# Performance work log

Hardware: AMD Instinct MI355X
Metric: run time of the kernel (lower is better)

The kernel has to match this reference:

```python
import jax, jax.numpy as jnp
import numpy as np

BLANK = 0
SIZE_AVERAGE = True


def rnnt_loss(acts, labels, act_lens, label_lens):
    # acts: (B, T, U+1, V) raw logits; warp-transducer applies log_softmax internally
    B, T, U1, V = acts.shape
    U = U1 - 1
    logp = jax.nn.log_softmax(acts, axis=-1)          # (B,T,U1,V)
    lp_blank = logp[..., BLANK]                       # (B,T,U1)
    # emission log-prob of label u at grid point (t,u): logp[b,t,u,labels[b,u]]
    lp_emit = jnp.take_along_axis(
        logp[:, :, :U, :], labels[:, None, :, None].astype(jnp.int32), axis=3
    )[..., 0]                                         # (B,T,U)

    # alpha[0,0]=0 ; alpha[0,u] = sum_{k<u} emit[0,k]
    row0 = jnp.concatenate(
        [jnp.zeros((B, 1), acts.dtype), jnp.cumsum(lp_emit[:, 0, :], axis=1)], axis=1
    )                                                 # (B,U1)

    def outer(prev_row, xs):
        blank_prev, emit_t = xs                       # (B,U1), (B,U)
        fb = prev_row + blank_prev                    # arrive via blank from t-1
        def inner(carry, x):
            fb_u, em_prev = x                         # (B,), (B,)
            a = jnp.logaddexp(fb_u, carry + em_prev)  # blank vs emit path
            return a, a
        _, rest = jax.lax.scan(inner, fb[:, 0], (fb[:, 1:].T, emit_t.T))  # (U,B)
        row = jnp.concatenate([fb[:, :1], rest.T], axis=1)               # (B,U1)
        return row, row

    xs = (jnp.moveaxis(lp_blank[:, :-1, :], 1, 0),   # (T-1,B,U1)
          jnp.moveaxis(lp_emit[:, 1:, :], 1, 0))     # (T-1,B,U)
    _, rows = jax.lax.scan(outer, row0, xs)          # (T-1,B,U1)
    alpha = jnp.concatenate([row0[None], rows], axis=0)  # (T,B,U1)

    b_idx = jnp.arange(B)
    t_idx = act_lens.astype(jnp.int32) - 1
    u_idx = label_lens.astype(jnp.int32)
    loglike = alpha[t_idx, b_idx, u_idx] + lp_blank[b_idx, t_idx, u_idx]
    total = -jnp.sum(loglike)
    if SIZE_AVERAGE:
        total = total / B
    return total.reshape(1)


def setup_inputs() -> dict:
    key = jax.random.key(0)
    k1, k2, k3, k4 = jax.random.split(key, 4)
    B, T, U, V = 8, 256, 100, 128
    acts = jax.random.normal(k1, (B, T, U + 1, V), dtype=jnp.float32)
    labels = jax.random.randint(k2, (B, U), 0, V, dtype=jnp.int64)
    act_lens = jax.random.randint(k3, (B,), T // 2, T + 1, dtype=jnp.int32)
    label_lens = jax.random.randint(k4, (B,), U // 2, U + 1, dtype=jnp.int32)
    return {"acts": acts, "labels": labels, "act_lens": act_lens, "label_lens": label_lens}


def reference(acts, labels, act_lens, label_lens):
    return rnnt_loss(acts, labels, act_lens, label_lens)
```

## Files before the change

### kernel.cpp

```cpp
#include <hip/hip_runtime.h>
#include <math.h>


#define B_DIM  8
#define T_DIM  256
#define U_DIM  100
#define U1_DIM 101
#define V_DIM  128

#define ROWU   128
#define DROWS  360
#define NEGF   (-8.0e29f)
#define LOG2E  1.4426950408889634f
#define LN2    0.69314718055994530942f

#define NITMAX 88
#define VROWU  320
#define VROWB  1280
#define LDS_BYTES (NITMAX * VROWB)

typedef unsigned uv2 __attribute__((ext_vector_type(2)));

__device__ __forceinline__ float ubit(unsigned u) { return __builtin_bit_cast(float, u); }
__device__ __forceinline__ float logadd2(float a, float b) {
    float m = fmaxf(a, b);
    float e = exp2f(-fabsf(a - b));
    return m + log2f(1.0f + e);
}
__device__ __forceinline__ float lse3(float a, float b, float c) {
    float m = fmaxf(fmaxf(a, b), c);
    float s = exp2f(a - m) + exp2f(b - m) + exp2f(c - m);
    return m + log2f(s);
}
__device__ __forceinline__ float lse5(float a, float b, float c, float d, float e) {
    float m = fmaxf(fmaxf(fmaxf(a, b), c), fmaxf(d, e));
    float s = exp2f(a - m) + exp2f(b - m) + exp2f(c - m) + exp2f(d - m) + exp2f(e - m);
    return m + log2f(s);
}
__device__ __forceinline__ float lane_shr1(float x) {
    int r = __builtin_amdgcn_update_dpp(0, __builtin_bit_cast(int, x),
                                        0x138 , 0xF, 0xF, true);
    return __builtin_bit_cast(float, r);
}
__device__ __forceinline__ unsigned f2bf(float f) {
    unsigned u = __builtin_bit_cast(unsigned, f);
    u += 0x7FFF + ((u >> 16) & 1);
    return u >> 16;
}

struct W2 { float tA, mA, lA, tB, mB, lB; };
__device__ __forceinline__ W2 buildW2m(uv2 c0, uv2 cm, int l, int d, int tl, int ul) {
    const int ua = 2 * l, ub = 2 * l + 1;
    float BL0a = ubit(c0.x << 16), EM0a = ubit(c0.x & 0xFFFF0000u);
    float BL0b = ubit(c0.y << 16), EM0b = ubit(c0.y & 0xFFFF0000u);
    float BLma = ubit(cm.x << 16), EMma = ubit(cm.x & 0xFFFF0000u);
    float BLmb = ubit(cm.y << 16), EMmb = ubit(cm.y & 0xFFFF0000u);
    BL0a = (ua <= ul && (unsigned)(d - 1 - ua) <= (unsigned)tl) ? BL0a : NEGF;
    BL0b = (ub <= ul && (unsigned)(d - 1 - ub) <= (unsigned)tl) ? BL0b : NEGF;
    EM0a = (ua >= 1 && ua <= ul && (unsigned)(d - ua) <= (unsigned)tl) ? EM0a : NEGF;
    EM0b = (ub <= ul && (unsigned)(d - ub) <= (unsigned)tl) ? EM0b : NEGF;
    BLma = (ua <= ul && (unsigned)(d - 2 - ua) <= (unsigned)tl) ? BLma : NEGF;
    BLmb = (ub <= ul && (unsigned)(d - 1 - ub) <= (unsigned)tl) ? BLmb : NEGF;
    EMma = (ua >= 1 && ua <= ul && (unsigned)(d - 1 - ua) <= (unsigned)tl) ? EMma : NEGF;
    EMmb = (ub <= ul && (unsigned)(d - 1 - ub) <= (unsigned)tl) ? EMmb : NEGF;
    float BLmp = lane_shr1(BLmb), EMmp = lane_shr1(EMmb);
    W2 w;
    w.tA = BLma + BL0a;
    w.mA = logadd2(EMma + BL0a, BLmp + EM0a);
    w.lA = EMmp + EM0a;
    w.tB = BLmb + BL0b;
    w.mB = logadd2(EMmb + BL0b, BLma + EM0b);
    w.lB = EMma + EM0b;
    if (l == 0) { w.mA = NEGF; w.lA = NEGF; w.lB = NEGF; }
    return w;
}

__device__ __forceinline__ void buildV4(const unsigned* combB, int dt, int l,
                                        int tl, int ul, float* out) {
    const unsigned* C = combB + (size_t)dt * ROWU + 2 * l;
    uv2 c0 = *(const uv2*)(C);
    uv2 c1 = *(const uv2*)(C - ROWU);
    uv2 c2 = *(const uv2*)(C - 2 * ROWU);
    uv2 c3 = *(const uv2*)(C - 3 * ROWU);
    W2 P = buildW2m(c0, c1, l, dt,     tl, ul);
    W2 Q = buildW2m(c2, c3, l, dt - 2, tl, ul);
    float Qt_b1 = lane_shr1(Q.tB), Qm_b1 = lane_shr1(Q.mB), Ql_b1 = lane_shr1(Q.lB);
    float Qt_a1 = lane_shr1(Q.tA), Qm_a1 = lane_shr1(Q.mA), Ql_a1 = lane_shr1(Q.lA);
    out[0] = P.tA + Q.tA;
    out[1] = logadd2(P.tA + Q.mA, P.mA + Qt_b1);
    out[2] = lse3(P.tA + Q.lA, P.mA + Qm_b1, P.lA + Qt_a1);
    out[3] = logadd2(P.mA + Ql_b1, P.lA + Qm_a1);
    out[4] = P.lA + Ql_a1;
    out[5] = P.tB + Q.tB;
    out[6] = logadd2(P.tB + Q.mB, P.mB + Q.tA);
    out[7] = lse3(P.tB + Q.lB, P.mB + Q.mA, P.lB + Qt_b1);
    out[8] = logadd2(P.mB + Q.lA, P.lB + Qm_b1);
    out[9] = P.lB + Ql_b1;
    if (l == 0) { out[1] = NEGF; out[2] = NEGF; out[3] = NEGF; out[4] = NEGF; }
}

__device__ __forceinline__ void prologue(const unsigned* combB, int start, int l,
                                         int tl, int ul, float& v0, float& v1) {
    v0 = (l == 0) ? 0.0f : NEGF;
    v1 = NEGF;
    for (int d = 1; d <= start; ++d) {
        uv2 c = *(const uv2*)(combB + (size_t)d * ROWU + 2 * l);
        const int ua = 2 * l, ub = 2 * l + 1;
        float bl0 = ubit(c.x << 16), em0 = ubit(c.x & 0xFFFF0000u);
        float bl1 = ubit(c.y << 16), em1 = ubit(c.y & 0xFFFF0000u);
        bl0 = (ua <= ul && (unsigned)(d - 1 - ua) <= (unsigned)tl) ? bl0 : NEGF;
        bl1 = (ub <= ul && (unsigned)(d - 1 - ub) <= (unsigned)tl) ? bl1 : NEGF;
        em0 = (ua >= 1 && ua <= ul && (unsigned)(d - ua) <= (unsigned)tl) ? em0 : NEGF;
        em1 = (ub <= ul && (unsigned)(d - ub) <= (unsigned)tl) ? em1 : NEGF;
        float left0 = lane_shr1(v1);
        float a0 = v0 + bl0, p0 = left0 + em0;
        float a1 = v1 + bl1, p1 = v0 + em1;
        v0 = logadd2(a0, p0);
        v1 = logadd2(a1, p1);
    }
}

__global__ __launch_bounds__(256) void lsm_kernel(
    const float* __restrict__ acts, const int* __restrict__ labels,
    const int* __restrict__ act_lens, const int* __restrict__ label_lens,
    unsigned short* __restrict__ comb, int* __restrict__ counter, int nrows)
{
    if (blockIdx.x == 0 && threadIdx.x == 0) *counter = 0;

    int rid = blockIdx.x * 8 + (threadIdx.x >> 5);
    if (rid >= nrows) return;
    int hl = threadIdx.x & 31;

    int u  = rid % U1_DIM;
    int bt = rid / U1_DIM;
    int b  = bt / T_DIM;
    int t  = bt - b * T_DIM;
    if (t >= act_lens[b] || u > label_lens[b]) return;

    const float* row = acts + (size_t)rid * V_DIM;
    float4 x = *reinterpret_cast<const float4*>(row + 4 * hl);
    float4 y = make_float4(x.x * LOG2E, x.y * LOG2E, x.z * LOG2E, x.w * LOG2E);

    float s = exp2f(y.x) + exp2f(y.y) + exp2f(y.z) + exp2f(y.w);
    #pragma unroll
    for (int off = 16; off; off >>= 1) s += __shfl_xor(s, off);
    float lse2 = log2f(s);

    unsigned short* C = comb + (size_t)b * DROWS * (ROWU * 2);
    int d = t + u + 1;
    if (hl == 0)
        C[(size_t)d * (ROWU * 2) + 2 * u] = (unsigned short)f2bf(y.x - lse2);
    if (u < U_DIM) {
        int lab = labels[b * U_DIM + u];
        if (hl == (lab >> 2)) {
            int r = lab & 3;
            float v = (r == 0) ? y.x : (r == 1) ? y.y : (r == 2) ? y.z : y.w;
            C[(size_t)d * (ROWU * 2) + 2 * u + 3] = (unsigned short)f2bf(v - lse2);
        }
    }
}

__global__ __launch_bounds__(256) void v4c_kernel(
    const unsigned* __restrict__ comb,
    const int* __restrict__ act_lens, const int* __restrict__ label_lens,
    unsigned* __restrict__ V)
{
    int wid = blockIdx.x * 4 + (threadIdx.x >> 6);
    if (wid >= B_DIM * NITMAX) return;
    int l  = threadIdx.x & 63;
    int b  = wid / NITMAX;
    int it = wid - b * NITMAX;

    int tl = act_lens[b] - 1, ul = label_lens[b];
    int dfin = tl + ul, start = dfin & 3, niter = dfin >> 2;
    if (it >= niter) return;
    int dt = start + 4 * (it + 1);

    float o[10];
    buildV4(comb + (size_t)b * DROWS * ROWU, dt, l, tl, ul, o);

    if (l < 52) {
        unsigned* ro = V + (size_t)(b * NITMAX + it) * VROWU;
        uv2 p0, p1, p2;
        p0.x = f2bf(o[0]) | (f2bf(o[1]) << 16); p0.y = f2bf(o[5]) | (f2bf(o[6]) << 16);
        p1.x = f2bf(o[2]) | (f2bf(o[3]) << 16); p1.y = f2bf(o[7]) | (f2bf(o[8]) << 16);
        p2.x = f2bf(o[4]);                      p2.y = f2bf(o[9]);
        __builtin_nontemporal_store(p0, (uv2*)(ro + 2 * l));
        __builtin_nontemporal_store(p1, (uv2*)(ro + 104 + 2 * l));
        __builtin_nontemporal_store(p2, (uv2*)(ro + 208 + 2 * l));
    }
}

__global__ __launch_bounds__(64, 1) void dp3_kernel(
    const unsigned* __restrict__ comb, const unsigned* __restrict__ V,
    const int* __restrict__ act_lens, const int* __restrict__ label_lens,
    float* __restrict__ loglike, int* __restrict__ counter,
    float* __restrict__ out)
{
    extern __shared__ char sV[];

    const int b = blockIdx.x;
    const int l = threadIdx.x;
    const int tl    = act_lens[b] - 1;
    const int ul    = label_lens[b];
    const int dfin  = tl + ul;
    const int start = dfin & 3;
    const int niter = dfin >> 2;

    const unsigned* combB = comb + (size_t)b * DROWS * ROWU;

    float fin_bl = ubit(combB[(size_t)(dfin + 1) * ROWU + ul] << 16);
    float v0, v1;
    prologue(combB, start, l, tl, ul, v0, v1);
    asm volatile("s_waitcnt vmcnt(0)" ::: "memory");

    {
        const char* g = (const char*)(V + (size_t)b * NITMAX * VROWU) + l * 16;
        const int nload = (niter * VROWB + 1023) >> 10;
        for (int i = 0; i < nload; ++i) {
            __builtin_amdgcn_global_load_lds(
                (const __attribute__((address_space(1))) void*)(g + (size_t)i * 1024),
                (__attribute__((address_space(3))) void*)(sV + (size_t)i * 1024), 16, 0, 0);
        }
        asm volatile("s_waitcnt vmcnt(0)" ::: "memory");
    }

    float rf0 = NEGF, rf1 = NEGF;
    const char* Lc = sV + 8 * l;
    uv2 q0[4], q1[4], q2[4];
    #pragma unroll
    for (int j = 0; j < 4; ++j) {
        const char* p = Lc + (size_t)j * VROWB;
        q0[j] = *(const uv2*)(p);
        q1[j] = *(const uv2*)(p + 416);
        q2[j] = *(const uv2*)(p + 832);
    }
    const int ngroups = (niter + 3) >> 2;
    for (int g4 = 0; g4 < ngroups; ++g4) {
        const int it0 = g4 * 4;
        #pragma unroll
        for (int J = 0; J < 4; ++J) {
            const int it = it0 + J;
            uv2 a0 = q0[J], a1 = q1[J], a2 = q2[J];
            float V0a = ubit(a0.x << 16), V1a = ubit(a0.x & 0xFFFF0000u);
            float V0b = ubit(a0.y << 16), V1b = ubit(a0.y & 0xFFFF0000u);
            float V2a = ubit(a1.x << 16), V3a = ubit(a1.x & 0xFFFF0000u);
            float V2b = ubit(a1.y << 16), V3b = ubit(a1.y & 0xFFFF0000u);
            float V4a = ubit(a2.x << 16), V4b = ubit(a2.y << 16);
            float s1 = lane_shr1(v1);
            float s0 = lane_shr1(v0);
            float s3 = lane_shr1(s1);
            float s2 = lane_shr1(s0);
            float nA = lse5(v0 + V0a, s1 + V1a, s0 + V2a, s3 + V3a, s2 + V4a);
            float nB = lse5(v1 + V0b, v0 + V1b, s1 + V2b, s0 + V3b, s3 + V4b);
            if (it == niter - 1) { rf0 = nA; rf1 = nB; }
            v0 = nA; v1 = nB;
            int rr = it + 4; rr = rr < niter ? rr : niter - 1;
            const char* p = Lc + (size_t)rr * VROWB;
            q0[J] = *(const uv2*)(p);
            q1[J] = *(const uv2*)(p + 416);
            q2[J] = *(const uv2*)(p + 832);
        }
    }

    float res = (ul & 1) ? rf1 : rf0;
    if (l == (ul >> 1)) {
        loglike[b] = LN2 * (res + fin_bl);
        __threadfence();
        int old = atomicAdd(counter, 1);
        if (old == B_DIM - 1) {
            __threadfence();
            float s = 0.0f;
            #pragma unroll
            for (int i = 0; i < B_DIM; ++i)
                s += __hip_atomic_load(&loglike[i], __ATOMIC_RELAXED,
                                       __HIP_MEMORY_SCOPE_AGENT);
            out[0] = -s / (float)B_DIM;
        }
    }
}

extern "C" void kernel_launch(void* const* d_in, const int* in_sizes, int n_in,
                              void* d_out, int out_size, void* d_ws, size_t ws_size,
                              hipStream_t stream) {
    const float* acts       = (const float*)d_in[0];
    const int*   labels     = (const int*)d_in[1];
    const int*   act_lens   = (const int*)d_in[2];
    const int*   label_lens = (const int*)d_in[3];

    unsigned* comb    = (unsigned*)d_ws;
    unsigned* V       = comb + (size_t)B_DIM * DROWS * ROWU;
    float*    loglike = (float*)(V + (size_t)B_DIM * NITMAX * VROWU);
    int*      counter = (int*)(loglike + B_DIM);

    int nrows   = B_DIM * T_DIM * U1_DIM;
    int nblocks = (nrows + 7) / 8;

    hipFuncSetAttribute(reinterpret_cast<const void*>(dp3_kernel),
                        hipFuncAttributeMaxDynamicSharedMemorySize, LDS_BYTES);

    lsm_kernel<<<nblocks, 256, 0, stream>>>(acts, labels, act_lens, label_lens,
                                            (unsigned short*)comb, counter, nrows);
    int vwaves = B_DIM * NITMAX;
    v4c_kernel<<<(vwaves + 3) / 4, 256, 0, stream>>>(comb, act_lens, label_lens, V);
    dp3_kernel<<<B_DIM, 64, LDS_BYTES, stream>>>(comb, V, act_lens, label_lens,
                                                 loglike, counter, (float*)d_out);
}
```

Baseline: 49.56 us.

## Fuse V-block construction into DP kernel via LDS, drop separate kernel

The separate v4c kernel that built per-iteration transfer blocks into global memory is removed. The DP kernel now runs with 1024 threads: 16 waves build those blocks straight into shared memory, then a single wave runs the serial recurrence after a barrier. This removes one kernel launch and a global-memory round trip. In exchange the block construction runs on only 8 workgroups instead of being spread across the whole GPU. The log-softmax stores also become nontemporal.

```diff
diff --git a/kernel.cpp b/kernel.cpp
--- a/kernel.cpp
+++ b/kernel.cpp
@@ -15,7 +15,6 @@
 #define LN2    0.69314718055994530942f
 
 #define NITMAX 88
-#define VROWU  320
 #define VROWB  1280
 #define LDS_BYTES (NITMAX * VROWB)
 
@@ -149,50 +148,21 @@
     unsigned short* C = comb + (size_t)b * DROWS * (ROWU * 2);
     int d = t + u + 1;
     if (hl == 0)
-        C[(size_t)d * (ROWU * 2) + 2 * u] = (unsigned short)f2bf(y.x - lse2);
+        __builtin_nontemporal_store((unsigned short)f2bf(y.x - lse2),
+                                    &C[(size_t)d * (ROWU * 2) + 2 * u]);
     if (u < U_DIM) {
         int lab = labels[b * U_DIM + u];
         if (hl == (lab >> 2)) {
             int r = lab & 3;
             float v = (r == 0) ? y.x : (r == 1) ? y.y : (r == 2) ? y.z : y.w;
-            C[(size_t)d * (ROWU * 2) + 2 * u + 3] = (unsigned short)f2bf(v - lse2);
-        }
-    }
-}
-
-__global__ __launch_bounds__(256) void v4c_kernel(
+            __builtin_nontemporal_store((unsigned short)f2bf(v - lse2),
+                                        &C[(size_t)d * (ROWU * 2) + 2 * u + 3]);
+        }
+    }
+}
+
+__global__ __launch_bounds__(1024, 1) void dp_kernel(
     const unsigned* __restrict__ comb,
-    const int* __restrict__ act_lens, const int* __restrict__ label_lens,
-    unsigned* __restrict__ V)
-{
-    int wid = blockIdx.x * 4 + (threadIdx.x >> 6);
-    if (wid >= B_DIM * NITMAX) return;
-    int l  = threadIdx.x & 63;
-    int b  = wid / NITMAX;
-    int it = wid - b * NITMAX;
-
-    int tl = act_lens[b] - 1, ul = label_lens[b];
-    int dfin = tl + ul, start = dfin & 3, niter = dfin >> 2;
-    if (it >= niter) return;
-    int dt = start + 4 * (it + 1);
-
-    float o[10];
-    buildV4(comb + (size_t)b * DROWS * ROWU, dt, l, tl, ul, o);
-
-    if (l < 52) {
-        unsigned* ro = V + (size_t)(b * NITMAX + it) * VROWU;
-        uv2 p0, p1, p2;
-        p0.x = f2bf(o[0]) | (f2bf(o[1]) << 16); p0.y = f2bf(o[5]) | (f2bf(o[6]) << 16);
-        p1.x = f2bf(o[2]) | (f2bf(o[3]) << 16); p1.y = f2bf(o[7]) | (f2bf(o[8]) << 16);
-        p2.x = f2bf(o[4]);                      p2.y = f2bf(o[9]);
-        __builtin_nontemporal_store(p0, (uv2*)(ro + 2 * l));
-        __builtin_nontemporal_store(p1, (uv2*)(ro + 104 + 2 * l));
-        __builtin_nontemporal_store(p2, (uv2*)(ro + 208 + 2 * l));
-    }
-}
-
-__global__ __launch_bounds__(64, 1) void dp3_kernel(
-    const unsigned* __restrict__ comb, const unsigned* __restrict__ V,
     const int* __restrict__ act_lens, const int* __restrict__ label_lens,
     float* __restrict__ loglike, int* __restrict__ counter,
     float* __restrict__ out)
@@ -200,7 +170,8 @@
     extern __shared__ char sV[];
 
     const int b = blockIdx.x;
-    const int l = threadIdx.x;
+    const int l = threadIdx.x & 63;
+    const int w = threadIdx.x >> 6;
     const int tl    = act_lens[b] - 1;
     const int ul    = label_lens[b];
     const int dfin  = tl + ul;
@@ -209,23 +180,29 @@
 
     const unsigned* combB = comb + (size_t)b * DROWS * ROWU;
 
+    for (int it = w; it < niter; it += 16) {
+        int dt = start + 4 * (it + 1);
+        float o[10];
+        buildV4(combB, dt, l, tl, ul, o);
+        if (l < 52) {
+            char* ro = sV + (size_t)it * VROWB + 8 * l;
+            uv2 p0, p1, p2;
+            p0.x = f2bf(o[0]) | (f2bf(o[1]) << 16); p0.y = f2bf(o[5]) | (f2bf(o[6]) << 16);
+            p1.x = f2bf(o[2]) | (f2bf(o[3]) << 16); p1.y = f2bf(o[7]) | (f2bf(o[8]) << 16);
+            p2.x = f2bf(o[4]);                      p2.y = f2bf(o[9]);
+            *(uv2*)(ro)       = p0;
+            *(uv2*)(ro + 416) = p1;
+            *(uv2*)(ro + 832) = p2;
+        }
+    }
+    __syncthreads();
+    if (w != 0) return;
+
     float fin_bl = ubit(combB[(size_t)(dfin + 1) * ROWU + ul] << 16);
     float v0, v1;
     prologue(combB, start, l, tl, ul, v0, v1);
-    asm volatile("s_waitcnt vmcnt(0)" ::: "memory");
-
-    {
-        const char* g = (const char*)(V + (size_t)b * NITMAX * VROWU) + l * 16;
-        const int nload = (niter * VROWB + 1023) >> 10;
-        for (int i = 0; i < nload; ++i) {
-            __builtin_amdgcn_global_load_lds(
-                (const __attribute__((address_space(1))) void*)(g + (size_t)i * 1024),
-                (__attribute__((address_space(3))) void*)(sV + (size_t)i * 1024), 16, 0, 0);
-        }
-        asm volatile("s_waitcnt vmcnt(0)" ::: "memory");
-    }
-
     float rf0 = NEGF, rf1 = NEGF;
+
     const char* Lc = sV + 8 * l;
     uv2 q0[4], q1[4], q2[4];
     #pragma unroll
@@ -289,20 +266,17 @@
     const int*   label_lens = (const int*)d_in[3];
 
     unsigned* comb    = (unsigned*)d_ws;
-    unsigned* V       = comb + (size_t)B_DIM * DROWS * ROWU;
-    float*    loglike = (float*)(V + (size_t)B_DIM * NITMAX * VROWU);
+    float*    loglike = (float*)(comb + (size_t)B_DIM * DROWS * ROWU);
     int*      counter = (int*)(loglike + B_DIM);
 
     int nrows   = B_DIM * T_DIM * U1_DIM;
     int nblocks = (nrows + 7) / 8;
 
-    hipFuncSetAttribute(reinterpret_cast<const void*>(dp3_kernel),
+    hipFuncSetAttribute(reinterpret_cast<const void*>(dp_kernel),
                         hipFuncAttributeMaxDynamicSharedMemorySize, LDS_BYTES);
 
     lsm_kernel<<<nblocks, 256, 0, stream>>>(acts, labels, act_lens, label_lens,
                                             (unsigned short*)comb, counter, nrows);
-    int vwaves = B_DIM * NITMAX;
-    v4c_kernel<<<(vwaves + 3) / 4, 256, 0, stream>>>(comb, act_lens, label_lens, V);
-    dp3_kernel<<<B_DIM, 64, LDS_BYTES, stream>>>(comb, V, act_lens, label_lens,
-                                                 loglike, counter, (float*)d_out);
-}
+    dp_kernel<<<B_DIM, 1024, LDS_BYTES, stream>>>(comb, act_lens, label_lens,
+                                                  loglike, counter, (float*)d_out);
+}
```

Result: slower. 80.38 us (+62.2%).
